# Kernel tuning notes

Measured on AMD Instinct MI355X. Metric: run time of the kernel, lower is better.

## Reference

```python
import jax, jax.numpy as jnp
import numpy as np

POOL = 7
H, W, C = 200, 200, 512
NUM_ROIS = 128


def setup_inputs() -> dict:
    key = jax.random.key(0)
    k1, k2, k3 = jax.random.split(key, 3)
    img = jax.random.normal(k1, (1, H, W, C), dtype=jnp.float32)
    # (x, y, w, h) in feature-map pixels; w,h >= POOL+1 so every bin is >=1px,
    # and x+w <= W, y+h <= H so crops stay in bounds (as the original assumes).
    wh = jax.random.uniform(k2, (1, NUM_ROIS, 2), minval=float(POOL + 1), maxval=64.0)
    xy = jax.random.uniform(k3, (1, NUM_ROIS, 2)) * (jnp.array([W, H], jnp.float32) - wh)
    rois = jnp.concatenate([xy, wh], axis=-1).astype(jnp.float32)
    return {"img": img, "rois": rois, "pool_size": POOL}


def _roi_pool(x, rois, P):
    # x: (H, W, C) feature map; rois: (R, 4) as (x, y, w, h) floats.
    h_dim, w_dim, _ = x.shape
    ks = jnp.arange(P + 1, dtype=jnp.float32)
    rows = jnp.arange(h_dim)
    cols = jnp.arange(w_dim)

    def pool_one(roi):
        rx, ry, rw, rh = roi[0], roi[1], roi[2], roi[3]
        # Bin boundaries: original computes x1 = int(x + ix*w/P), x2 = int(x + (ix+1)*w/P),
        # i.e. contiguous non-overlapping segments [b[k], b[k+1]).
        bx = (rx + ks * (rw / P)).astype(jnp.int32)
        by = (ry + ks * (rh / P)).astype(jnp.int32)
        # Map each row/col to its bin id; out-of-roi pixels -> dummy segment P.
        rid = jnp.searchsorted(by, rows, side='right') - 1
        rid = jnp.where((rid < 0) | (rid >= P), P, rid)
        cid = jnp.searchsorted(bx, cols, side='right') - 1
        cid = jnp.where((cid < 0) | (cid >= P), P, cid)
        # Max-reduce rows into y-bins, then cols into x-bins (separable rect max).
        rm = jax.ops.segment_max(x, rid, num_segments=P + 1)                     # (P+1, W, C) [jy, w, c]
        cm = jax.ops.segment_max(rm.transpose(1, 0, 2), cid, num_segments=P + 1)  # (P+1, P+1, C) [ix, jy, c]
        return cm[:P, :P].transpose(1, 0, 2)  # (jy, ix, c)

    return jax.vmap(pool_one)(rois)  # (R, P, P, C)


def reference(img, rois, pool_size):
    # Output: (1, num_rois, pool_size, pool_size, channels), tf dim ordering.
    out = _roi_pool(img[0], rois[0], pool_size)
    return out[None]
```

## Files before the change

### kernel.cpp

```cpp
#include <hip/hip_runtime.h>


#define IMG_H 200
#define IMG_W 200
#define IMG_C 512
#define POOL 7
#define NROI 128

__global__ __launch_bounds__(128) void roi_pool_kernel(
    const float* __restrict__ img,
    const float* __restrict__ rois,
    float* __restrict__ out)
{
    const int bin = blockIdx.x % (POOL * POOL);
    const int roi = blockIdx.x / (POOL * POOL);
    const int jy = bin / POOL;
    const int ix = bin % POOL;

    const float rx = rois[roi * 4 + 0];
    const float ry = rois[roi * 4 + 1];
    const float rw = rois[roi * 4 + 2];
    const float rh = rois[roi * 4 + 3];

    const float sx = __fdiv_rn(rw, 7.0f);
    const float sy = __fdiv_rn(rh, 7.0f);
    const int x1 = (int)__fadd_rn(rx, __fmul_rn((float)ix,       sx));
    const int x2 = (int)__fadd_rn(rx, __fmul_rn((float)(ix + 1), sx));
    const int y1 = (int)__fadd_rn(ry, __fmul_rn((float)jy,       sy));
    const int y2 = (int)__fadd_rn(ry, __fmul_rn((float)(jy + 1), sy));

    const int c4 = threadIdx.x;
    const float4* __restrict__ img4 = (const float4*)img;

    float4 m = make_float4(-INFINITY, -INFINITY, -INFINITY, -INFINITY);
    for (int y = y1; y < y2; ++y) {
        const float4* __restrict__ row = img4 + ((size_t)y * IMG_W) * (IMG_C / 4) + c4;
        for (int x = x1; x < x2; ++x) {
            float4 v = row[(size_t)x * (IMG_C / 4)];
            m.x = fmaxf(m.x, v.x);
            m.y = fmaxf(m.y, v.y);
            m.z = fmaxf(m.z, v.z);
            m.w = fmaxf(m.w, v.w);
        }
    }

    float4* __restrict__ out4 = (float4*)out;
    out4[((size_t)(roi * POOL + jy) * POOL + ix) * (IMG_C / 4) + c4] = m;
}

extern "C" void kernel_launch(void* const* d_in, const int* in_sizes, int n_in,
                              void* d_out, int out_size, void* d_ws, size_t ws_size,
                              hipStream_t stream) {
    (void)in_sizes; (void)n_in; (void)d_ws; (void)ws_size; (void)out_size;
    const float* img  = (const float*)d_in[0];
    const float* rois = (const float*)d_in[1];
    float* out = (float*)d_out;

    dim3 grid(NROI * POOL * POOL);
    dim3 block(128);
    roi_pool_kernel<<<grid, block, 0, stream>>>(img, rois, out);
}
```

Measured before the change: 152.7 us.

## Unroll bin loop 4x2 with clamped loads, remap blocks per XCD, set occupancy

Changes the inner bin max loop to read a 4-row by 2-column tile per iteration into eight independent accumulators. Indices are clamped to the last row and column so edge cases need no branches, at the cost of some duplicate loads. This gives more memory-level parallelism per thread. It also remaps block indices so each of the 8 XCDs handles a contiguous group of ROIs to improve L2 locality, and adds a min-blocks hint of 4 to launch_bounds.

```diff
diff --git a/kernel.cpp b/kernel.cpp
--- a/kernel.cpp
+++ b/kernel.cpp
@@ -4,16 +4,25 @@
 #define IMG_H 200
 #define IMG_W 200
 #define IMG_C 512
+#define C4 (IMG_C / 4)
 #define POOL 7
 #define NROI 128
 
-__global__ __launch_bounds__(128) void roi_pool_kernel(
+__device__ __forceinline__ float4 max4(float4 a, float4 b) {
+    return make_float4(fmaxf(a.x, b.x), fmaxf(a.y, b.y),
+                       fmaxf(a.z, b.z), fmaxf(a.w, b.w));
+}
+
+__global__ __launch_bounds__(128, 4) void roi_pool_kernel(
     const float* __restrict__ img,
     const float* __restrict__ rois,
     float* __restrict__ out)
 {
-    const int bin = blockIdx.x % (POOL * POOL);
-    const int roi = blockIdx.x / (POOL * POOL);
+    const int b     = blockIdx.x;
+    const int xcd   = b & 7;
+    const int local = b >> 3;
+    const int roi   = xcd * (NROI / 8) + local / (POOL * POOL);
+    const int bin   = local % (POOL * POOL);
     const int jy = bin / POOL;
     const int ix = bin % POOL;
 
@@ -29,23 +38,61 @@
     const int y1 = (int)__fadd_rn(ry, __fmul_rn((float)jy,       sy));
     const int y2 = (int)__fadd_rn(ry, __fmul_rn((float)(jy + 1), sy));
 
+    const int x2m1 = x2 - 1;
+    const int y2m1 = y2 - 1;
+    const int nr = (y2 - y1 + 3) >> 2;
+    const int nc = (x2 - x1 + 1) >> 1;
+
     const int c4 = threadIdx.x;
-    const float4* __restrict__ img4 = (const float4*)img;
+    const float4* __restrict__ img4 = (const float4*)img + c4;
 
-    float4 m = make_float4(-INFINITY, -INFINITY, -INFINITY, -INFINITY);
-    for (int y = y1; y < y2; ++y) {
-        const float4* __restrict__ row = img4 + ((size_t)y * IMG_W) * (IMG_C / 4) + c4;
-        for (int x = x1; x < x2; ++x) {
-            float4 v = row[(size_t)x * (IMG_C / 4)];
-            m.x = fmaxf(m.x, v.x);
-            m.y = fmaxf(m.y, v.y);
-            m.z = fmaxf(m.z, v.z);
-            m.w = fmaxf(m.w, v.w);
+    float4 ninf = make_float4(-INFINITY, -INFINITY, -INFINITY, -INFINITY);
+    float4 m0 = ninf, m1 = ninf, m2 = ninf, m3 = ninf;
+    float4 m4 = ninf, m5 = ninf, m6 = ninf, m7 = ninf;
+
+    for (int r = 0; r < nr; ++r) {
+        const int yb = y1 + 4 * r;
+        const int ya0 = min(yb,     y2m1);
+        const int ya1 = min(yb + 1, y2m1);
+        const int ya2 = min(yb + 2, y2m1);
+        const int ya3 = min(yb + 3, y2m1);
+        const float4* __restrict__ p0 = img4 + (size_t)ya0 * (IMG_W * C4);
+        const float4* __restrict__ p1 = img4 + (size_t)ya1 * (IMG_W * C4);
+        const float4* __restrict__ p2 = img4 + (size_t)ya2 * (IMG_W * C4);
+        const float4* __restrict__ p3 = img4 + (size_t)ya3 * (IMG_W * C4);
+        for (int k = 0; k < nc; ++k) {
+            const int xa = min(x1 + 2 * k,     x2m1);
+            const int xb = min(x1 + 2 * k + 1, x2m1);
+            const size_t oa = (size_t)xa * C4;
+            const size_t ob = (size_t)xb * C4;
+            float4 v0 = p0[oa];
+            float4 v1 = p0[ob];
+            float4 v2 = p1[oa];
+            float4 v3 = p1[ob];
+            float4 v4 = p2[oa];
+            float4 v5 = p2[ob];
+            float4 v6 = p3[oa];
+            float4 v7 = p3[ob];
+            m0 = max4(m0, v0);
+            m1 = max4(m1, v1);
+            m2 = max4(m2, v2);
+            m3 = max4(m3, v3);
+            m4 = max4(m4, v4);
+            m5 = max4(m5, v5);
+            m6 = max4(m6, v6);
+            m7 = max4(m7, v7);
         }
     }
+    m0 = max4(m0, m1);
+    m2 = max4(m2, m3);
+    m4 = max4(m4, m5);
+    m6 = max4(m6, m7);
+    m0 = max4(m0, m2);
+    m4 = max4(m4, m6);
+    m0 = max4(m0, m4);
 
     float4* __restrict__ out4 = (float4*)out;
-    out4[((size_t)(roi * POOL + jy) * POOL + ix) * (IMG_C / 4) + c4] = m;
+    out4[((size_t)(roi * (POOL * POOL) + bin)) * C4 + c4] = m0;
 }
 
 extern "C" void kernel_launch(void* const* d_in, const int* in_sizes, int n_in,
```

Measured after the change: 147.8 us. 1.03x faster.

## Double-buffer bin pixel loads via global_load_lds async copies into LDS

Applied to the files above, without the earlier changes.

Replaces the direct per-pixel global float4 loads with asynchronous global-to-LDS loads (global_load_lds), issued in chunks of 8 pixels and double-buffered per wave, with waitcnt-based synchronisation. Chunk tails are padded by repeating the last pixel so max stays correct. The goal is to keep more memory requests in flight and overlap load latency with the max reductions. In exchange it adds LDS traffic, hand-coded waitcnt encodings and per-wave LDS buffers that can reduce occupancy.

```diff
diff --git a/kernel.cpp b/kernel.cpp
--- a/kernel.cpp
+++ b/kernel.cpp
@@ -1,4 +1,5 @@
 #include <hip/hip_runtime.h>
+#include <stdint.h>
 
 
 #define IMG_H 200
@@ -6,12 +7,27 @@
 #define IMG_C 512
 #define POOL 7
 #define NROI 128
+#define CHUNK 8
+
+#define AS1(p) ((const __attribute__((address_space(1))) void*)(p))
+#define AS3(p) ((__attribute__((address_space(3))) void*)(p))
+
+__device__ __forceinline__ float4 max4(float4 a, float4 b) {
+    return make_float4(fmaxf(a.x, b.x), fmaxf(a.y, b.y),
+                       fmaxf(a.z, b.z), fmaxf(a.w, b.w));
+}
 
 __global__ __launch_bounds__(128) void roi_pool_kernel(
     const float* __restrict__ img,
     const float* __restrict__ rois,
     float* __restrict__ out)
 {
+    __shared__ float lds[2 * 2 * CHUNK * 64 * 4];
+
+    const int tid  = threadIdx.x;
+    const int wv   = tid >> 6;
+    const int lane = tid & 63;
+
     const int bin = blockIdx.x % (POOL * POOL);
     const int roi = blockIdx.x / (POOL * POOL);
     const int jy = bin / POOL;
@@ -29,23 +45,57 @@
     const int y1 = (int)__fadd_rn(ry, __fmul_rn((float)jy,       sy));
     const int y2 = (int)__fadd_rn(ry, __fmul_rn((float)(jy + 1), sy));
 
-    const int c4 = threadIdx.x;
-    const float4* __restrict__ img4 = (const float4*)img;
+    const int nx = x2 - x1;
+    const int ny = y2 - y1;
+    const int n  = nx * ny;
+    const int nchunks = (n + CHUNK - 1) / CHUNK;
 
-    float4 m = make_float4(-INFINITY, -INFINITY, -INFINITY, -INFINITY);
-    for (int y = y1; y < y2; ++y) {
-        const float4* __restrict__ row = img4 + ((size_t)y * IMG_W) * (IMG_C / 4) + c4;
-        for (int x = x1; x < x2; ++x) {
-            float4 v = row[(size_t)x * (IMG_C / 4)];
-            m.x = fmaxf(m.x, v.x);
-            m.y = fmaxf(m.y, v.y);
-            m.z = fmaxf(m.z, v.z);
-            m.w = fmaxf(m.w, v.w);
+    const char* gbase = (const char*)img + (size_t)tid * 16;
+    float* ldsw = lds + wv * (2 * CHUNK * 256);
+
+    int px = 0, py = 0;
+
+    auto issue_chunk = [&](int buf) {
+        float* lb = ldsw + buf * (CHUNK * 256);
+        #pragma unroll
+        for (int s = 0; s < CHUNK; ++s) {
+            const char* gp = gbase +
+                (size_t)((y1 + py) * IMG_W + (x1 + px)) * (IMG_C * 4);
+            __builtin_amdgcn_global_load_lds(AS1(gp), AS3(lb + s * 256), 16, 0, 0);
+            if (++px == nx) { px = 0; if (++py == ny) { py = ny - 1; px = nx - 1; } }
         }
+    };
+
+    issue_chunk(0);
+
+    float4 m0 = make_float4(-INFINITY, -INFINITY, -INFINITY, -INFINITY);
+    float4 m1 = m0;
+
+    for (int c = 0; c < nchunks; ++c) {
+        const int buf = c & 1;
+        const bool more = (c + 1 < nchunks);
+        if (more) {
+            issue_chunk(buf ^ 1);
+            __builtin_amdgcn_s_waitcnt(0x0F78);
+        } else {
+            __builtin_amdgcn_s_waitcnt(0x0F70);
+        }
+        __builtin_amdgcn_sched_barrier(0);
+
+        const float* lb = ldsw + buf * (CHUNK * 256) + lane * 4;
+        #pragma unroll
+        for (int s = 0; s < CHUNK; s += 2) {
+            float4 v0 = *(const float4*)(lb + (s + 0) * 256);
+            float4 v1 = *(const float4*)(lb + (s + 1) * 256);
+            m0 = max4(m0, v0);
+            m1 = max4(m1, v1);
+        }
+        __builtin_amdgcn_sched_barrier(0);
     }
+    m0 = max4(m0, m1);
 
     float4* __restrict__ out4 = (float4*)out;
-    out4[((size_t)(roi * POOL + jy) * POOL + ix) * (IMG_C / 4) + c4] = m;
+    out4[((size_t)(roi * (POOL * POOL) + bin)) * (IMG_C / 4) + tid] = m0;
 }
 
 extern "C" void kernel_launch(void* const* d_in, const int* in_sizes, int n_in,
```

Result: faster. 143.3 us (-6.1%).
